# Kernel optimization log

Hardware: AMD Instinct MI355X
Metric: run time of the kernel (lower is better)

The kernel has to match this reference:

```python
import jax, jax.numpy as jnp
import numpy as np

N, E, G, IN, H, L, C = 20000, 320000, 128, 16, 64, 4, 10
AVG_D_LOG = float(np.log(17.0))  # log(avg_degree + 1)


def setup_inputs() -> dict:
    key = jax.random.key(0)
    ks = jax.random.split(key, 24)
    p = lambda k, shape: jax.random.normal(k, shape, dtype=jnp.float32) * 0.05
    return dict(
        h=jax.random.normal(ks[0], (N, IN), jnp.float32),
        snorm_n=jax.random.uniform(ks[1], (N, 1), jnp.float32, 0.05, 1.0),
        embW=p(ks[2], (IN, H)), embB=p(ks[3], (H,)),
        preW=p(ks[4], (L, 2 * H, H)), preB=p(ks[5], (L, H)),
        postW=p(ks[6], (L, 13 * H, H)), postB=p(ks[7], (L, H)),
        mixW=p(ks[8], (L, H, H)), mixB=p(ks[9], (L, H)),
        r1W=p(ks[10], (H, H // 2)), r1B=p(ks[11], (H // 2,)),
        r2W=p(ks[12], (H // 2, H // 4)), r2B=p(ks[13], (H // 4,)),
        r3W=p(ks[14], (H // 4, C)), r3B=p(ks[15], (C,)),
        src=jax.random.randint(ks[16], (E,), 0, N),
        dst=jax.random.randint(ks[17], (E,), 0, N),
        graph_ids=jnp.sort(jax.random.randint(ks[18], (N,), 0, G)),
    )


def _pna_forward(h, snorm_n, embW, embB, preW, preB, postW, postB, mixW, mixB,
                 r1W, r1B, r2W, r2B, r3W, r3B, src, dst, graph_ids):
    # Degree-based scalers (computed once; graph is fixed across layers)
    deg = jax.ops.segment_sum(jnp.ones((E,), h.dtype), dst, num_segments=N)  # [N]
    degc = jnp.maximum(deg, 1.0)[:, None]
    logd = jnp.log(deg + 1.0)
    amp = (logd / AVG_D_LOG)[:, None]                      # amplification scaler
    att = (AVG_D_LOG / jnp.maximum(logd, 1e-5))[:, None]   # attenuation scaler
    has_nb = (deg > 0.0)[:, None]

    x = h @ embW + embB  # node embedding [N, H]
    for i in range(L):
        x_in = x
        # pretrans: per-edge message from cat(h_src, h_dst)  [E, H]
        m = jnp.concatenate([x[src], x[dst]], axis=-1) @ preW[i] + preB[i]
        # multi-aggregator reduce at dst: mean, max, min, std
        mean = jax.ops.segment_sum(m, dst, num_segments=N) / degc
        msq = jax.ops.segment_sum(m * m, dst, num_segments=N) / degc
        std = jnp.sqrt(jax.nn.relu(msq - mean * mean) + 1e-5)
        mx = jnp.where(has_nb, jax.ops.segment_max(m, dst, num_segments=N), 0.0)
        mn = jnp.where(has_nb, jax.ops.segment_min(m, dst, num_segments=N), 0.0)
        agg = jnp.concatenate([mean, mx, mn, std], axis=-1)  # [N, 4H]
        # degree scalers: identity, amplification, attenuation -> [N, 12H]
        scaled = jnp.concatenate([agg, agg * amp, agg * att], axis=-1)
        # posttrans over cat(scaled_agg, h) -> [N, H]
        y = jnp.concatenate([scaled, x], axis=-1) @ postW[i] + postB[i]
        # tower mixing network (LeakyReLU FC)
        y = jax.nn.leaky_relu(y @ mixW[i] + mixB[i])
        y = y * snorm_n          # graph norm
        x = x_in + y             # residual
    # mean-nodes readout per graph
    gsum = jax.ops.segment_sum(x, graph_ids, num_segments=G)
    cnt = jnp.maximum(jax.ops.segment_sum(jnp.ones((N,), x.dtype), graph_ids, num_segments=G), 1.0)
    hg = gsum / cnt[:, None]
    # MLPReadout: two halving ReLU layers + classifier
    hg = jax.nn.relu(hg @ r1W + r1B)
    hg = jax.nn.relu(hg @ r2W + r2B)
    return hg @ r3W + r3B  # [G, C]


def reference(h, snorm_n, embW, embB, preW, preB, postW, postB, mixW, mixB,
              r1W, r1B, r2W, r2B, r3W, r3B, src, dst, graph_ids):
    return _pna_forward(h, snorm_n, embW, embB, preW, preB, postW, postB,
                        mixW, mixB, r1W, r1B, r2W, r2B, r3W, r3B,
                        src, dst, graph_ids)
```

## Files before the change

kernel.cpp:

```cpp
#include <hip/hip_runtime.h>
#include <math.h>

#define N_ 20000
#define E_ 320000
#define G_ 128
#define IN_ 16
#define H_ 64
#define L_ 4
#define C_ 10
#define AVG_D_LOG 2.8332133440562162f

union F4 { float4 v; float f[4]; };

typedef _Float16 h8 __attribute__((ext_vector_type(8)));
typedef _Float16 h4 __attribute__((ext_vector_type(4)));
typedef float f4x __attribute__((ext_vector_type(4)));
#define MFMA16(a, b, c) __builtin_amdgcn_mfma_f32_16x16x32_f16((a), (b), (c), 0, 0, 0)


__global__ __launch_bounds__(256) void k_setup(
    const float* __restrict__ h, const float* __restrict__ embW, const float* __restrict__ embB,
    float* __restrict__ x,
    const float* __restrict__ preW, const float* __restrict__ postW, const float* __restrict__ mixW,
    _Float16* __restrict__ preWT, _Float16* __restrict__ postWT, _Float16* __restrict__ mixWT,
    int* __restrict__ zbase) {
  int bb = blockIdx.x, tid = threadIdx.x;
  if (bb < 5000) {
    int n = bb * 4 + (tid >> 6);
    int c = tid & 63;
    float acc = embB[c];
#pragma unroll
    for (int k = 0; k < IN_; k++) acc += h[n * IN_ + k] * embW[k * H_ + c];
    x[n * H_ + c] = acc;
  } else if (bb < 6024) {
    int idx = (bb - 5000) * 256 + tid;
    if (idx < 32768) {
      int l = idx >> 13, r = idx & 8191;
      int c = r >> 6, k = r & 63;
      preWT[idx] = (_Float16)preW[l * 8192 + k * 64 + c];
    } else if (idx < 245760) {
      int j = idx - 32768;
      int l = j / 53248, r = j % 53248;
      int c = r / 832, k = r % 832;
      postWT[j] = (_Float16)postW[l * 53248 + k * 64 + c];
    } else {
      int j = idx - 245760;
      int l = j >> 12, r = j & 4095;
      int c = r >> 6, k = r & 63;
      mixWT[j] = (_Float16)mixW[l * 4096 + k * 64 + c];
    }
  } else {
    int i = (bb - 6024) * 256 + tid;
    if (i < 2 * N_) zbase[i] = 0;
  }
}


__global__ __launch_bounds__(256) void k_hist(const int* __restrict__ dst, int* __restrict__ deg) {
  int e = blockIdx.x * 256 + threadIdx.x;
  if (e < E_) atomicAdd(&deg[dst[e]], 1);
}


__global__ __launch_bounds__(1024) void k_scan(const int* __restrict__ deg, int* __restrict__ offs) {
  __shared__ int sh[1024];
  int t = threadIdx.x;
  int base = t * 20;
  int local[20];
  int s = 0;
#pragma unroll
  for (int i = 0; i < 20; i++) {
    int idx = base + i;
    int v = (idx < N_) ? deg[idx] : 0;
    local[i] = s; s += v;
  }
  sh[t] = s;
  __syncthreads();
  for (int off = 1; off < 1024; off <<= 1) {
    int v = (t >= off) ? sh[t - off] : 0;
    __syncthreads();
    sh[t] += v;
    __syncthreads();
  }
  int excl = sh[t] - s;
#pragma unroll
  for (int i = 0; i < 20; i++) {
    int idx = base + i;
    if (idx < N_) offs[idx] = excl + local[i];
  }
  if (t == 0) offs[N_] = sh[1023];
}


__global__ __launch_bounds__(256) void k_mix(
    const int* __restrict__ src, const int* __restrict__ dst,
    const int* __restrict__ offs, int* __restrict__ cursor, int* __restrict__ csr,
    const int* __restrict__ deg,
    float* __restrict__ ampv, float* __restrict__ attv,
    float* __restrict__ invd, float* __restrict__ hnb,
    const float* __restrict__ x, const _Float16* __restrict__ preWT,
    const float* __restrict__ preB, _Float16* __restrict__ ah, float* __restrict__ b) {
  int bb = blockIdx.x, tid = threadIdx.x;
  if (bb < 1250) {
    int e = bb * 256 + tid;
    if (e < E_) {
      int d = dst[e];
      int pos = offs[d] + atomicAdd(&cursor[d], 1);
      csr[pos] = src[e];
    }
  } else if (bb < 1329) {
    int idx = (bb - 1250) * 256 + tid;
    if (idx < N_) {
      float d = (float)deg[idx];
      float logd = logf(d + 1.f);
      ampv[idx] = logd / AVG_D_LOG;
      attv[idx] = AVG_D_LOG / fmaxf(logd, 1e-5f);
      invd[idx] = 1.f / fmaxf(d, 1.f);
      hnb[idx] = d > 0.f ? 1.f : 0.f;
    }
  } else {
    int n0 = (bb - 1329) * 32;
    int lane = tid & 63, wv = tid >> 6;
    int mt = wv & 1, nh = wv >> 1;
    int l15 = lane & 15, k0q = (lane >> 4) * 8;
    int mrow = n0 + mt * 16 + l15;
    const float* xr = x + (size_t)mrow * 64;
    const _Float16* wb0 = preWT + (size_t)(nh * 64 + l15) * 64 + k0q;
    f4x acc0 = {0.f,0.f,0.f,0.f}, acc1 = {0.f,0.f,0.f,0.f}, acc2 = {0.f,0.f,0.f,0.f}, acc3 = {0.f,0.f,0.f,0.f};
#pragma unroll
    for (int kb = 0; kb < 64; kb += 32) {
      int ko = kb + k0q;
      F4 xa, xb2;
      xa.v = *(const float4*)(xr + ko);
      xb2.v = *(const float4*)(xr + ko + 4);
      h8 af;
      af[0]=(_Float16)xa.f[0]; af[1]=(_Float16)xa.f[1]; af[2]=(_Float16)xa.f[2]; af[3]=(_Float16)xa.f[3];
      af[4]=(_Float16)xb2.f[0]; af[5]=(_Float16)xb2.f[1]; af[6]=(_Float16)xb2.f[2]; af[7]=(_Float16)xb2.f[3];
      acc0 = MFMA16(af, *(const h8*)(wb0 + kb), acc0);
      acc1 = MFMA16(af, *(const h8*)(wb0 + 1024 + kb), acc1);
      acc2 = MFMA16(af, *(const h8*)(wb0 + 2048 + kb), acc2);
      acc3 = MFMA16(af, *(const h8*)(wb0 + 3072 + kb), acc3);
    }
    int rbase = n0 + mt * 16 + (lane >> 4) * 4;
    f4x accs[4] = {acc0, acc1, acc2, acc3};
#pragma unroll
    for (int t = 0; t < 4; t++) {
      int col = nh * 64 + t * 16 + l15;
#pragma unroll
      for (int r = 0; r < 4; r++) {
        int n = rbase + r;
        if (col < 64) ah[(size_t)n * 64 + col] = (_Float16)accs[t][r];
        else          b[(size_t)n * 64 + (col - 64)] = accs[t][r] + preB[col - 64];
      }
    }
  }
}


__global__ __launch_bounds__(256) void k_layer(
    const _Float16* __restrict__ ahin, const float* __restrict__ bin,
    const int* __restrict__ offs, const int* __restrict__ csr,
    const float* __restrict__ invd, const float* __restrict__ hnb,
    const _Float16* __restrict__ WT, const float* __restrict__ Bv,
    const _Float16* __restrict__ mixWT, const float* __restrict__ mixB,
    const float* __restrict__ ampv, const float* __restrict__ attv,
    const float* __restrict__ snorm, float* __restrict__ x,
    const _Float16* __restrict__ preWT, const float* __restrict__ preB,
    _Float16* __restrict__ ahout, float* __restrict__ bout, int do_pre) {
  __shared__ _Float16 aggs[16 * 272];
  __shared__ _Float16 ys[16 * 80];
  __shared__ _Float16 xs[16 * 80];
  int tid = threadIdx.x;
  int n0 = blockIdx.x * 16;
  int lane = tid & 63, wv = tid >> 6;

  {
    int nl = tid >> 4, q = tid & 15;
    int n = n0 + nl;
    int o0 = offs[n];
    int deg = offs[n + 1] - o0;
    float sum[4], sq[4], mx[4], mn[4];
#pragma unroll
    for (int i = 0; i < 4; i++) {
      sum[i] = 0.f; sq[i] = 0.f;
      mx[i] = -__builtin_inff(); mn[i] = __builtin_inff();
    }
    int j = 0;
    for (; j + 3 < deg; j += 4) {
      int s0 = csr[o0 + j];
      int s1 = csr[o0 + j + 1];
      int s2 = csr[o0 + j + 2];
      int s3 = csr[o0 + j + 3];
      h4 a0 = *(const h4*)(ahin + (size_t)s0 * 64 + q * 4);
      h4 a1 = *(const h4*)(ahin + (size_t)s1 * 64 + q * 4);
      h4 a2 = *(const h4*)(ahin + (size_t)s2 * 64 + q * 4);
      h4 a3 = *(const h4*)(ahin + (size_t)s3 * 64 + q * 4);
#pragma unroll
      for (int i = 0; i < 4; i++) {
        float v0 = (float)a0[i], v1 = (float)a1[i], v2 = (float)a2[i], v3 = (float)a3[i];
        sum[i] += (v0 + v1) + (v2 + v3);
        sq[i] += v0 * v0;
        sq[i] += v1 * v1;
        sq[i] += v2 * v2;
        sq[i] += v3 * v3;
        mx[i] = fmaxf(mx[i], fmaxf(fmaxf(v0, v1), fmaxf(v2, v3)));
        mn[i] = fminf(mn[i], fminf(fminf(v0, v1), fminf(v2, v3)));
      }
    }
    for (; j < deg; j++) {
      int s0 = csr[o0 + j];
      h4 a0 = *(const h4*)(ahin + (size_t)s0 * 64 + q * 4);
#pragma unroll
      for (int i = 0; i < 4; i++) {
        float v0 = (float)a0[i];
        sum[i] += v0;
        sq[i] += v0 * v0;
        mx[i] = fmaxf(mx[i], v0);
        mn[i] = fminf(mn[i], v0);
      }
    }
    float inv = invd[n], hn = hnb[n];
    F4 bv; bv.v = *(const float4*)(bin + (size_t)n * 64 + q * 4);
    h4 hm, hx, hmn, hs;
#pragma unroll
    for (int i = 0; i < 4; i++) {
      float mean_a = sum[i] * inv;
      float var = sq[i] * inv - mean_a * mean_a;
      hs[i] = (_Float16)sqrtf(fmaxf(var, 0.f) + 1e-5f);
      bool nb = hn > 0.5f;
      hm[i] = (_Float16)(nb ? (mean_a + bv.f[i]) : 0.f);
      hx[i] = (_Float16)(nb ? (mx[i] + bv.f[i]) : 0.f);
      hmn[i] = (_Float16)(nb ? (mn[i] + bv.f[i]) : 0.f);
    }
    _Float16* ap = aggs + nl * 272 + q * 4;
    *(h4*)(ap) = hm;
    *(h4*)(ap + 64) = hx;
    *(h4*)(ap + 128) = hmn;
    *(h4*)(ap + 192) = hs;
  }
  __syncthreads();

  int nh = wv;
  int l15 = lane & 15, k0q = (lane >> 4) * 8;
  int mrow = n0 + l15;
  const _Float16* ag = aggs + (size_t)l15 * 272 + k0q;
  int col0 = nh * 16 + l15;
  const _Float16* w0 = WT + (size_t)col0 * 832 + k0q;
  f4x aI = {0.f,0.f,0.f,0.f}, aA = {0.f,0.f,0.f,0.f}, aT = {0.f,0.f,0.f,0.f};
#pragma unroll 4
  for (int kb = 0; kb < 256; kb += 32) {
    h8 af = *(const h8*)(ag + kb);
    aI = MFMA16(af, *(const h8*)(w0 + kb), aI);
    aA = MFMA16(af, *(const h8*)(w0 + 256 + kb), aA);
    aT = MFMA16(af, *(const h8*)(w0 + 512 + kb), aT);
  }
  const float* xr = x + (size_t)mrow * 64;
#pragma unroll
  for (int kb = 0; kb < 64; kb += 32) {
    int ko = kb + k0q;
    F4 xa, xb2;
    xa.v = *(const float4*)(xr + ko);
    xb2.v = *(const float4*)(xr + ko + 4);
    h8 af;
    af[0]=(_Float16)xa.f[0]; af[1]=(_Float16)xa.f[1]; af[2]=(_Float16)xa.f[2]; af[3]=(_Float16)xa.f[3];
    af[4]=(_Float16)xb2.f[0]; af[5]=(_Float16)xb2.f[1]; af[6]=(_Float16)xb2.f[2]; af[7]=(_Float16)xb2.f[3];
    aI = MFMA16(af, *(const h8*)(w0 + 768 + kb), aI);
  }
  int qr = (lane >> 4) * 4;
  int rbase = n0 + qr;
  int yrow = qr;
  float b0 = Bv[col0];
#pragma unroll
  for (int r = 0; r < 4; r++) {
    int n = rbase + r;
    float amp = ampv[n], att = attv[n];
    ys[(yrow + r) * 80 + col0] = (_Float16)(aI[r] + b0 + amp * aA[r] + att * aT[r]);
  }
  __syncthreads();
  f4x m0 = {0.f,0.f,0.f,0.f};
  const _Float16* yr = ys + (size_t)l15 * 80 + k0q;
  const _Float16* mw0 = mixWT + (size_t)col0 * 64 + k0q;
#pragma unroll
  for (int kb = 0; kb < 64; kb += 32) {
    h8 af = *(const h8*)(yr + kb);
    m0 = MFMA16(af, *(const h8*)(mw0 + kb), m0);
  }
  float mb0 = mixB[col0];
#pragma unroll
  for (int r = 0; r < 4; r++) {
    int n = rbase + r;
    float sn = snorm[n];
    float t0 = m0[r] + mb0; t0 = t0 > 0.f ? t0 : 0.01f * t0;
    float* xp = x + (size_t)n * 64;
    float xo0 = xp[col0] + t0 * sn;
    xp[col0] = xo0;
    xs[(yrow + r) * 80 + col0] = (_Float16)xo0;
  }

  if (do_pre) {
    __syncthreads();
    int ch = wv;
    const _Float16* xf = xs + (size_t)l15 * 80 + k0q;
    const _Float16* wb0 = preWT + (size_t)(ch * 32 + l15) * 64 + k0q;
    f4x p0 = {0.f,0.f,0.f,0.f}, p1 = {0.f,0.f,0.f,0.f};
#pragma unroll
    for (int kb = 0; kb < 64; kb += 32) {
      h8 af = *(const h8*)(xf + kb);
      p0 = MFMA16(af, *(const h8*)(wb0 + kb), p0);
      p1 = MFMA16(af, *(const h8*)(wb0 + 1024 + kb), p1);
    }
    int prb = n0 + (lane >> 4) * 4;
    f4x accs[2] = {p0, p1};
#pragma unroll
    for (int t = 0; t < 2; t++) {
      int col = ch * 32 + t * 16 + l15;
#pragma unroll
      for (int r = 0; r < 4; r++) {
        int n = prb + r;
        if (col < 64) ahout[(size_t)n * 64 + col] = (_Float16)accs[t][r];
        else          bout[(size_t)n * 64 + (col - 64)] = accs[t][r] + preB[col - 64];
      }
    }
  }
}


__device__ inline int lower_bound_gid(const int* __restrict__ gid, int val) {
  int lo = 0, hi = N_;
  while (lo < hi) {
    int mid = (lo + hi) >> 1;
    if (gid[mid] < val) lo = mid + 1; else hi = mid;
  }
  return lo;
}

__global__ __launch_bounds__(256) void k_readout_fused(
    const float* __restrict__ x, const int* __restrict__ gid,
    const float* __restrict__ r1W, const float* __restrict__ r1B,
    const float* __restrict__ r2W, const float* __restrict__ r2B,
    const float* __restrict__ r3W, const float* __restrict__ r3B,
    float* __restrict__ out) {
  __shared__ float part[4 * 64];
  __shared__ float hg[64];
  __shared__ float t1[32];
  __shared__ float t2[16];
  int g = blockIdx.x, tid = threadIdx.x;
  int lo = lower_bound_gid(gid, g);
  int hi = lower_bound_gid(gid, g + 1);
  int c = tid & 63, w = tid >> 6;
  float s = 0.f;
  for (int n = lo + w; n < hi; n += 4) s += x[(size_t)n * 64 + c];
  part[w * 64 + c] = s;
  __syncthreads();
  if (w == 0) {
    float tot = part[c] + part[64 + c] + part[128 + c] + part[192 + c];
    float cnt = (float)(hi - lo);
    if (cnt < 1.f) cnt = 1.f;
    hg[c] = tot / cnt;
  }
  __syncthreads();
  if (tid < 32) {
    float acc = r1B[tid];
#pragma unroll 8
    for (int k = 0; k < 64; k++) acc += hg[k] * r1W[k * 32 + tid];
    t1[tid] = fmaxf(acc, 0.f);
  }
  __syncthreads();
  if (tid < 16) {
    float acc = r2B[tid];
#pragma unroll 8
    for (int k = 0; k < 32; k++) acc += t1[k] * r2W[k * 16 + tid];
    t2[tid] = fmaxf(acc, 0.f);
  }
  __syncthreads();
  if (tid < 10) {
    float acc = r3B[tid];
#pragma unroll
    for (int k = 0; k < 16; k++) acc += t2[k] * r3W[k * 10 + tid];
    out[g * 10 + tid] = acc;
  }
}


extern "C" void kernel_launch(void* const* d_in, const int* in_sizes, int n_in,
                              void* d_out, int out_size, void* d_ws, size_t ws_size,
                              hipStream_t stream) {
  const float* h     = (const float*)d_in[0];
  const float* snorm = (const float*)d_in[1];
  const float* embW  = (const float*)d_in[2];
  const float* embB  = (const float*)d_in[3];
  const float* preW  = (const float*)d_in[4];
  const float* preB  = (const float*)d_in[5];
  const float* postW = (const float*)d_in[6];
  const float* postB = (const float*)d_in[7];
  const float* mixW  = (const float*)d_in[8];
  const float* mixB  = (const float*)d_in[9];
  const float* r1W   = (const float*)d_in[10];
  const float* r1B   = (const float*)d_in[11];
  const float* r2W   = (const float*)d_in[12];
  const float* r2B   = (const float*)d_in[13];
  const float* r3W   = (const float*)d_in[14];
  const float* r3B   = (const float*)d_in[15];
  const int* src     = (const int*)d_in[16];
  const int* dst     = (const int*)d_in[17];
  const int* gid     = (const int*)d_in[18];
  float* out = (float*)d_out;

  char* w = (char*)d_ws;
  float* x        = (float*)w; w += (size_t)N_ * 64 * 4;
  _Float16* ah0   = (_Float16*)w; w += (size_t)N_ * 64 * 2;
  _Float16* ah1   = (_Float16*)w; w += (size_t)N_ * 64 * 2;
  float* b0       = (float*)w; w += (size_t)N_ * 64 * 4;
  float* b1       = (float*)w; w += (size_t)N_ * 64 * 4;
  _Float16* preWT = (_Float16*)w; w += (size_t)4 * 128 * 64 * 2;
  _Float16* postWT= (_Float16*)w; w += (size_t)4 * 64 * 832 * 2;
  _Float16* mixWT = (_Float16*)w; w += (size_t)4 * 64 * 64 * 2;
  float* ampv = (float*)w; w += (size_t)N_ * 4;
  float* attv = (float*)w; w += (size_t)N_ * 4;
  float* invd = (float*)w; w += (size_t)N_ * 4;
  float* hnb  = (float*)w; w += (size_t)N_ * 4;
  int* csr    = (int*)w;   w += (size_t)E_ * 4;
  int* offs   = (int*)w;   w += (size_t)(N_ + 64) * 4;
  int* zbase  = (int*)w;
  int* deg    = (int*)w;   w += (size_t)N_ * 4;
  int* cursor = (int*)w;   w += (size_t)N_ * 4;

  k_setup<<<6181, 256, 0, stream>>>(h, embW, embB, x, preW, postW, mixW,
                                    preWT, postWT, mixWT, zbase);
  k_hist<<<E_ / 256, 256, 0, stream>>>(dst, deg);
  k_scan<<<1, 1024, 0, stream>>>(deg, offs);
  k_mix<<<1250 + 79 + 625, 256, 0, stream>>>(src, dst, offs, cursor, csr, deg,
                                             ampv, attv, invd, hnb,
                                             x, preWT, preB, ah0, b0);
  int gb = N_ / 16;
  _Float16* ahs[2] = {ah0, ah1};
  float* bs[2] = {b0, b1};
  for (int l = 0; l < L_; l++) {
    int pin = l & 1, pout = 1 - pin;
    k_layer<<<gb, 256, 0, stream>>>(ahs[pin], bs[pin], offs, csr, invd, hnb,
                                    postWT + (size_t)l * 53248, postB + l * H_,
                                    mixWT + (size_t)l * 4096, mixB + l * H_,
                                    ampv, attv, snorm, x,
                                    preWT + (size_t)(l + 1 < L_ ? l + 1 : 0) * 8192,
                                    preB + (l + 1 < L_ ? l + 1 : 0) * H_,
                                    ahs[pout], bs[pout], l + 1 < L_ ? 1 : 0);
  }
  k_readout_fused<<<G_, 256, 0, stream>>>(x, gid, r1W, r1B, r2W, r2B, r3W, r3B, out);
}
```

Baseline: 300.8 us.

## Stage CSR slice, offsets and fp16 x tile in LDS; pad LDS rows; vectorize scan

The layer kernel now cooperatively loads each block's CSR neighbour slice (up to 1024 edges), its node offsets and an fp16 copy of its x rows into shared memory up front. The gather loop then reads indices from LDS instead of global memory, and the posttrans x operand comes from LDS instead of per-lane float loads plus conversion. LDS row strides are padded to reduce bank conflicts, launch bounds request 4 blocks per CU, and the scan kernel uses int4 vector loads and stores. This costs more shared memory and an extra barrier, and blocks with more than 1024 edges fall back to the global CSR path.

```diff
diff --git a/kernel.cpp b/kernel.cpp
--- a/kernel.cpp
+++ b/kernel.cpp
@@ -68,11 +68,15 @@
   int base = t * 20;
   int local[20];
   int s = 0;
-#pragma unroll
-  for (int i = 0; i < 20; i++) {
-    int idx = base + i;
-    int v = (idx < N_) ? deg[idx] : 0;
-    local[i] = s; s += v;
+  if (t < 1000) {
+#pragma unroll
+    for (int c = 0; c < 5; c++) {
+      int4 v = *(const int4*)(deg + base + c * 4);
+      local[c * 4 + 0] = s; s += v.x;
+      local[c * 4 + 1] = s; s += v.y;
+      local[c * 4 + 2] = s; s += v.z;
+      local[c * 4 + 3] = s; s += v.w;
+    }
   }
   sh[t] = s;
   __syncthreads();
@@ -82,11 +86,17 @@
     sh[t] += v;
     __syncthreads();
   }
-  int excl = sh[t] - s;
-#pragma unroll
-  for (int i = 0; i < 20; i++) {
-    int idx = base + i;
-    if (idx < N_) offs[idx] = excl + local[i];
+  if (t < 1000) {
+    int excl = sh[t] - s;
+#pragma unroll
+    for (int c = 0; c < 5; c++) {
+      int4 o;
+      o.x = excl + local[c * 4 + 0];
+      o.y = excl + local[c * 4 + 1];
+      o.z = excl + local[c * 4 + 2];
+      o.w = excl + local[c * 4 + 3];
+      *(int4*)(offs + base + c * 4) = o;
+    }
   }
   if (t == 0) offs[N_] = sh[1023];
 }
@@ -157,7 +167,7 @@
 }
 
 
-__global__ __launch_bounds__(256) void k_layer(
+__global__ __launch_bounds__(256, 4) void k_layer(
     const _Float16* __restrict__ ahin, const float* __restrict__ bin,
     const int* __restrict__ offs, const int* __restrict__ csr,
     const float* __restrict__ invd, const float* __restrict__ hnb,
@@ -167,60 +177,93 @@
     const float* __restrict__ snorm, float* __restrict__ x,
     const _Float16* __restrict__ preWT, const float* __restrict__ preB,
     _Float16* __restrict__ ahout, float* __restrict__ bout, int do_pre) {
-  __shared__ _Float16 aggs[16 * 272];
-  __shared__ _Float16 ys[16 * 80];
-  __shared__ _Float16 xs[16 * 80];
+  __shared__ _Float16 aggs[16 * 280];
+  __shared__ _Float16 ys[16 * 88];
+  __shared__ _Float16 xs[16 * 88];
+  __shared__ _Float16 xt[16 * 72];
+  __shared__ int csr_s[1024];
+  __shared__ int soffs[17];
   int tid = threadIdx.x;
   int n0 = blockIdx.x * 16;
   int lane = tid & 63, wv = tid >> 6;
 
+  int e0 = offs[n0];
+  int ecnt = offs[n0 + 16] - e0;
+  {
+    int row = tid >> 4, qq = tid & 15;
+    F4 xv; xv.v = *(const float4*)(x + (size_t)(n0 + row) * 64 + qq * 4);
+    h4 xh;
+    xh[0] = (_Float16)xv.f[0]; xh[1] = (_Float16)xv.f[1];
+    xh[2] = (_Float16)xv.f[2]; xh[3] = (_Float16)xv.f[3];
+    *(h4*)(xt + row * 72 + qq * 4) = xh;
+  }
+  if (tid < 17) soffs[tid] = offs[n0 + tid];
+  {
+    int cnt = ecnt < 1024 ? ecnt : 1024;
+    for (int i = tid; i < cnt; i += 256) csr_s[i] = csr[e0 + i];
+  }
+  __syncthreads();
+
   {
     int nl = tid >> 4, q = tid & 15;
     int n = n0 + nl;
-    int o0 = offs[n];
-    int deg = offs[n + 1] - o0;
+    int o0 = soffs[nl];
+    int deg = soffs[nl + 1] - o0;
+    float inv = invd[n], hn = hnb[n];
+    F4 bv; bv.v = *(const float4*)(bin + (size_t)n * 64 + q * 4);
     float sum[4], sq[4], mx[4], mn[4];
 #pragma unroll
     for (int i = 0; i < 4; i++) {
       sum[i] = 0.f; sq[i] = 0.f;
       mx[i] = -__builtin_inff(); mn[i] = __builtin_inff();
     }
-    int j = 0;
-    for (; j + 3 < deg; j += 4) {
-      int s0 = csr[o0 + j];
-      int s1 = csr[o0 + j + 1];
-      int s2 = csr[o0 + j + 2];
-      int s3 = csr[o0 + j + 3];
-      h4 a0 = *(const h4*)(ahin + (size_t)s0 * 64 + q * 4);
-      h4 a1 = *(const h4*)(ahin + (size_t)s1 * 64 + q * 4);
-      h4 a2 = *(const h4*)(ahin + (size_t)s2 * 64 + q * 4);
-      h4 a3 = *(const h4*)(ahin + (size_t)s3 * 64 + q * 4);
-#pragma unroll
-      for (int i = 0; i < 4; i++) {
-        float v0 = (float)a0[i], v1 = (float)a1[i], v2 = (float)a2[i], v3 = (float)a3[i];
-        sum[i] += (v0 + v1) + (v2 + v3);
-        sq[i] += v0 * v0;
-        sq[i] += v1 * v1;
-        sq[i] += v2 * v2;
-        sq[i] += v3 * v3;
-        mx[i] = fmaxf(mx[i], fmaxf(fmaxf(v0, v1), fmaxf(v2, v3)));
-        mn[i] = fminf(mn[i], fminf(fminf(v0, v1), fminf(v2, v3)));
+#define ACC4_(S0, S1, S2, S3)                                            \
+    do {                                                                 \
+      h4 a0 = *(const h4*)(ahin + (size_t)(S0) * 64 + q * 4);            \
+      h4 a1 = *(const h4*)(ahin + (size_t)(S1) * 64 + q * 4);            \
+      h4 a2 = *(const h4*)(ahin + (size_t)(S2) * 64 + q * 4);            \
+      h4 a3 = *(const h4*)(ahin + (size_t)(S3) * 64 + q * 4);            \
+      _Pragma("unroll")                                                  \
+      for (int i = 0; i < 4; i++) {                                      \
+        float v0 = (float)a0[i], v1 = (float)a1[i];                      \
+        float v2 = (float)a2[i], v3 = (float)a3[i];                      \
+        sum[i] += (v0 + v1) + (v2 + v3);                                 \
+        sq[i] += v0 * v0; sq[i] += v1 * v1;                              \
+        sq[i] += v2 * v2; sq[i] += v3 * v3;                              \
+        mx[i] = fmaxf(mx[i], fmaxf(fmaxf(v0, v1), fmaxf(v2, v3)));       \
+        mn[i] = fminf(mn[i], fminf(fminf(v0, v1), fminf(v2, v3)));       \
+      }                                                                  \
+    } while (0)
+#define ACC1_(S0)                                                        \
+    do {                                                                 \
+      h4 a0 = *(const h4*)(ahin + (size_t)(S0) * 64 + q * 4);            \
+      _Pragma("unroll")                                                  \
+      for (int i = 0; i < 4; i++) {                                      \
+        float v0 = (float)a0[i];                                         \
+        sum[i] += v0; sq[i] += v0 * v0;                                  \
+        mx[i] = fmaxf(mx[i], v0); mn[i] = fminf(mn[i], v0);              \
+      }                                                                  \
+    } while (0)
+    if (ecnt <= 1024) {
+      int lo = o0 - e0;
+      int j = 0;
+      for (; j + 3 < deg; j += 4) {
+        int s0 = csr_s[lo + j], s1 = csr_s[lo + j + 1];
+        int s2 = csr_s[lo + j + 2], s3 = csr_s[lo + j + 3];
+        ACC4_(s0, s1, s2, s3);
       }
-    }
-    for (; j < deg; j++) {
-      int s0 = csr[o0 + j];
-      h4 a0 = *(const h4*)(ahin + (size_t)s0 * 64 + q * 4);
-#pragma unroll
-      for (int i = 0; i < 4; i++) {
-        float v0 = (float)a0[i];
-        sum[i] += v0;
-        sq[i] += v0 * v0;
-        mx[i] = fmaxf(mx[i], v0);
-        mn[i] = fminf(mn[i], v0);
+      for (; j < deg; j++) { int s0 = csr_s[lo + j]; ACC1_(s0); }
+    } else {
+      int j = 0;
+      for (; j + 3 < deg; j += 4) {
+        int s0 = csr[o0 + j], s1 = csr[o0 + j + 1];
+        int s2 = csr[o0 + j + 2], s3 = csr[o0 + j + 3];
+        ACC4_(s0, s1, s2, s3);
       }
-    }
-    float inv = invd[n], hn = hnb[n];
-    F4 bv; bv.v = *(const float4*)(bin + (size_t)n * 64 + q * 4);
+      for (; j < deg; j++) { int s0 = csr[o0 + j]; ACC1_(s0); }
+    }
+#undef ACC4_
+#undef ACC1_
     h4 hm, hx, hmn, hs;
 #pragma unroll
     for (int i = 0; i < 4; i++) {
@@ -232,7 +275,7 @@
       hx[i] = (_Float16)(nb ? (mx[i] + bv.f[i]) : 0.f);
       hmn[i] = (_Float16)(nb ? (mn[i] + bv.f[i]) : 0.f);
     }
-    _Float16* ap = aggs + nl * 272 + q * 4;
+    _Float16* ap = aggs + nl * 280 + q * 4;
     *(h4*)(ap) = hm;
     *(h4*)(ap + 64) = hx;
     *(h4*)(ap + 128) = hmn;
@@ -242,8 +285,7 @@
 
   int nh = wv;
   int l15 = lane & 15, k0q = (lane >> 4) * 8;
-  int mrow = n0 + l15;
-  const _Float16* ag = aggs + (size_t)l15 * 272 + k0q;
+  const _Float16* ag = aggs + (size_t)l15 * 280 + k0q;
   int col0 = nh * 16 + l15;
   const _Float16* w0 = WT + (size_t)col0 * 832 + k0q;
   f4x aI = {0.f,0.f,0.f,0.f}, aA = {0.f,0.f,0.f,0.f}, aT = {0.f,0.f,0.f,0.f};
@@ -254,16 +296,10 @@
     aA = MFMA16(af, *(const h8*)(w0 + 256 + kb), aA);
     aT = MFMA16(af, *(const h8*)(w0 + 512 + kb), aT);
   }
-  const float* xr = x + (size_t)mrow * 64;
+  const _Float16* xtr = xt + (size_t)l15 * 72 + k0q;
 #pragma unroll
   for (int kb = 0; kb < 64; kb += 32) {
-    int ko = kb + k0q;
-    F4 xa, xb2;
-    xa.v = *(const float4*)(xr + ko);
-    xb2.v = *(const float4*)(xr + ko + 4);
-    h8 af;
-    af[0]=(_Float16)xa.f[0]; af[1]=(_Float16)xa.f[1]; af[2]=(_Float16)xa.f[2]; af[3]=(_Float16)xa.f[3];
-    af[4]=(_Float16)xb2.f[0]; af[5]=(_Float16)xb2.f[1]; af[6]=(_Float16)xb2.f[2]; af[7]=(_Float16)xb2.f[3];
+    h8 af = *(const h8*)(xtr + kb);
     aI = MFMA16(af, *(const h8*)(w0 + 768 + kb), aI);
   }
   int qr = (lane >> 4) * 4;
@@ -274,11 +310,11 @@
   for (int r = 0; r < 4; r++) {
     int n = rbase + r;
     float amp = ampv[n], att = attv[n];
-    ys[(yrow + r) * 80 + col0] = (_Float16)(aI[r] + b0 + amp * aA[r] + att * aT[r]);
+    ys[(yrow + r) * 88 + col0] = (_Float16)(aI[r] + b0 + amp * aA[r] + att * aT[r]);
   }
   __syncthreads();
   f4x m0 = {0.f,0.f,0.f,0.f};
-  const _Float16* yr = ys + (size_t)l15 * 80 + k0q;
+  const _Float16* yr = ys + (size_t)l15 * 88 + k0q;
   const _Float16* mw0 = mixWT + (size_t)col0 * 64 + k0q;
 #pragma unroll
   for (int kb = 0; kb < 64; kb += 32) {
@@ -294,13 +330,13 @@
     float* xp = x + (size_t)n * 64;
     float xo0 = xp[col0] + t0 * sn;
     xp[col0] = xo0;
-    xs[(yrow + r) * 80 + col0] = (_Float16)xo0;
+    xs[(yrow + r) * 88 + col0] = (_Float16)xo0;
   }
 
   if (do_pre) {
     __syncthreads();
     int ch = wv;
-    const _Float16* xf = xs + (size_t)l15 * 80 + k0q;
+    const _Float16* xf = xs + (size_t)l15 * 88 + k0q;
     const _Float16* wb0 = preWT + (size_t)(ch * 32 + l15) * 64 + k0q;
     f4x p0 = {0.f,0.f,0.f,0.f}, p1 = {0.f,0.f,0.f,0.f};
 #pragma unroll
```

After: 277.5 us. 1.08x faster.
